# Kernel tuning notes

Measured on AMD Instinct MI355X. Metric: run time of the kernel, lower is better.

## Reference

```python
import jax, jax.numpy as jnp
import numpy as np

N = 100000      # nodes
E = 3200000     # edges
F_IN = 128      # num_features
H = 32          # hidden_dim (hard-coded in module)
C = 8           # num_classes
B = 128         # graphs in batch
BN_EPS = 1e-5


def setup_inputs() -> dict:
    key = jax.random.key(0)
    ks = jax.random.split(key, 24)
    s = 0.1
    inp = {
        "x": jax.random.normal(ks[0], (N, F_IN), jnp.float32),
        "edge_index": jax.random.randint(ks[1], (2, E), 0, N, dtype=jnp.int32),
        "batch": jnp.sort(jax.random.randint(ks[2], (N,), 0, B, dtype=jnp.int32)),
        # GINConv layer 0 (F_IN -> H -> H) MLP + BN params
        "w1_0": jax.random.normal(ks[3], (F_IN, H), jnp.float32) * s,
        "b1_0": jnp.zeros((H,), jnp.float32),
        "w2_0": jax.random.normal(ks[4], (H, H), jnp.float32) * s,
        "b2_0": jnp.zeros((H,), jnp.float32),
        "g_0": jnp.ones((H,), jnp.float32),
        "be_0": jnp.zeros((H,), jnp.float32),
        # GINConv layers 1..3 (H -> H -> H), stacked
        "w1s": jax.random.normal(ks[5], (3, H, H), jnp.float32) * s,
        "b1s": jnp.zeros((3, H), jnp.float32),
        "w2s": jax.random.normal(ks[6], (3, H, H), jnp.float32) * s,
        "b2s": jnp.zeros((3, H), jnp.float32),
        "gs": jnp.ones((3, H), jnp.float32),
        "bes": jnp.zeros((3, H), jnp.float32),
        # classifier head
        "fc1_w": jax.random.normal(ks[7], (H, H), jnp.float32) * s,
        "fc1_b": jnp.zeros((H,), jnp.float32),
        "fc2_w": jax.random.normal(ks[8], (H, C), jnp.float32) * s,
        "fc2_b": jnp.zeros((C,), jnp.float32),
    }
    return inp


def _gin_conv(h, src, dst, w1, b1, w2, b2):
    # GINConv with eps=0: MLP((1+eps)*x + sum_{j in N(i)} x_j)
    agg = jax.ops.segment_sum(h[src], dst, num_segments=N)  # scatter-add aggregation
    z = h + agg
    return jnp.maximum(z @ w1 + b1, 0.0) @ w2 + b2


def _batch_norm(h, gamma, beta):
    # BatchNorm1d in training mode: batch stats over node dim, biased variance
    mean = h.mean(axis=0)
    var = jnp.mean(jnp.square(h - mean), axis=0)
    return gamma * (h - mean) * jax.lax.rsqrt(var + BN_EPS) + beta


def reference(x, edge_index, batch, w1_0, b1_0, w2_0, b2_0, g_0, be_0,
              w1s, b1s, w2s, b2s, gs, bes, fc1_w, fc1_b, fc2_w, fc2_b):
    src, dst = edge_index[0], edge_index[1]
    h = _batch_norm(jnp.maximum(_gin_conv(x, src, dst, w1_0, b1_0, w2_0, b2_0), 0.0), g_0, be_0)
    for i in range(3):  # fixed small layer loop
        h = _batch_norm(jnp.maximum(_gin_conv(h, src, dst, w1s[i], b1s[i], w2s[i], b2s[i]), 0.0), gs[i], bes[i])
    # global_mean_pool over batch ids
    counts = jax.ops.segment_sum(jnp.ones((N,), h.dtype), batch, num_segments=B)
    pooled = jax.ops.segment_sum(h, batch, num_segments=B) / jnp.maximum(counts, 1.0)[:, None]
    h = jnp.maximum(pooled @ fc1_w + fc1_b, 0.0)
    # dropout p=0.5 treated as identity (eval-mode determinism)
    logits = h @ fc2_w + fc2_b
    return jax.nn.log_softmax(logits, axis=-1)
```

## Files before the change

### kernel.cpp

```cpp
#include <hip/hip_runtime.h>
#include <hip/hip_bf16.h>

#define NN   100000
#define EE   3200000
#define HH   32
#define BB   128
#define KMAX 96
#define LSTRIDE 97
#define NBKT 1024
#define BSPAN 98
#define EBLK 256
#define CHUNK 12500

typedef float f32x4 __attribute__((ext_vector_type(4)));

static constexpr size_t Q_OFF      = 0;
static constexpr size_t EPACK_OFF  = 6400000;
static constexpr size_t H_OFF      = 19200000;
static constexpr size_t SRC_OFF    = 32000000;
static constexpr size_t OFF_OFF    = 44800000;
static constexpr size_t HIST_OFF   = 45300000;
static constexpr size_t CUR_OFF    = 46400000;
static constexpr size_t BBASE_OFF  = 47500000;
static constexpr size_t STATS_OFF  = 47600000;
static constexpr size_t POOLED_OFF = 47601024;
static constexpr size_t PCNT_OFF   = 47617408;
static constexpr size_t TOTAL_OFF  = 47617920;
static constexpr size_t ZERO_OFF   = STATS_OFF;
static constexpr size_t ZERO_BYTES = 22016;

__global__ __launch_bounds__(256) void hist_kernel(const int* __restrict__ ei,
                                                   int* __restrict__ hist,
                                                   int* __restrict__ total) {
    __shared__ int lh[NBKT];
    int tid = threadIdx.x, blk = blockIdx.x;
    for (int i = tid; i < NBKT; i += 256) lh[i] = 0;
    __syncthreads();
    int e0 = blk * CHUNK;
    for (int e = e0 + tid; e < e0 + CHUNK; e += 256) {
        int d = ei[EE + e];
        atomicAdd(&lh[d / BSPAN], 1);
    }
    __syncthreads();
    for (int i = tid; i < NBKT; i += 256) {
        int c = lh[i];
        hist[blk * NBKT + i] = c;
        if (c > 0) atomicAdd(&total[i], c);
    }
}

__global__ __launch_bounds__(1024) void bucket_scan_kernel(const int* __restrict__ total,
                                                           int* __restrict__ bbase,
                                                           int* __restrict__ cursor) {
    __shared__ int sm[NBKT];
    int t = threadIdx.x;
    int mine = total[t];
    sm[t] = mine;
    __syncthreads();
    for (int off = 1; off < NBKT; off <<= 1) {
        int v = (t >= off) ? sm[t - off] : 0;
        __syncthreads();
        sm[t] += v;
        __syncthreads();
    }
    int base = sm[t] - mine;
    bbase[t] = base;
    cursor[t] = base;
    if (t == NBKT - 1) bbase[NBKT] = sm[t];
}

__global__ __launch_bounds__(256) void scatter_kernel(const int* __restrict__ ei,
                                                      const int* __restrict__ hist,
                                                      int* __restrict__ cursor,
                                                      int* __restrict__ epack) {
    __shared__ int lbs[NBKT];
    __shared__ int lh[NBKT];
    int tid = threadIdx.x, blk = blockIdx.x;
    for (int i = tid; i < NBKT; i += 256) {
        int c = hist[blk * NBKT + i];
        lbs[i] = (c > 0) ? atomicAdd(&cursor[i], c) : 0;
        lh[i] = 0;
    }
    __syncthreads();
    int e0 = blk * CHUNK;
    for (int e = e0 + tid; e < e0 + CHUNK; e += 256) {
        int s = ei[e];
        int d = ei[EE + e];
        int b = d / BSPAN;
        int slot = lbs[b] + atomicAdd(&lh[b], 1);
        epack[slot] = s | ((d - b * BSPAN) << 17);
    }
}

__global__ __launch_bounds__(256) void csr_compact_kernel(const int* __restrict__ epack,
                                                          const int* __restrict__ bbase,
                                                          int* __restrict__ off,
                                                          int* __restrict__ srcs) {
    __shared__ int lcnt[BSPAN];
    __shared__ int lbase[BSPAN + 1];
    __shared__ int lcsr[BSPAN * LSTRIDE];
    int b = blockIdx.x;
    int base = b * BSPAN;
    int span = NN - base;
    if (span <= 0) return;
    if (span > BSPAN) span = BSPAN;
    int tid = threadIdx.x;
    for (int i = tid; i < span; i += 256) lcnt[i] = 0;
    __syncthreads();
    int p0 = bbase[b], p1 = bbase[b + 1];
    for (int i = p0 + tid; i < p1; i += 256) {
        int wd = epack[i];
        int ld = wd >> 17;
        int slot = atomicAdd(&lcnt[ld], 1);
        if (slot < KMAX) lcsr[ld * LSTRIDE + slot] = wd & 0x1FFFF;
    }
    __syncthreads();
    if (tid == 0) {
        int run = 0;
        for (int i = 0; i < span; i++) { lbase[i] = run; run += min(lcnt[i], KMAX); }
        lbase[span] = run;
    }
    __syncthreads();
    for (int i = tid; i < span; i += 256) off[base + i] = p0 + lbase[i];
    if (base + span == NN && tid == 0) off[NN] = p0 + lbase[span];
    int m = lbase[span];
    for (int j = tid; j < m; j += 256) {
        int lo = 0, hi = span - 1;
        while (lo < hi) {
            int mid = (lo + hi + 1) >> 1;
            if (lbase[mid] <= j) lo = mid; else hi = mid - 1;
        }
        srcs[p0 + j] = lcsr[lo * LSTRIDE + (j - lbase[lo])];
    }
}

__device__ __forceinline__ unsigned bf16rn(float f) {
    unsigned b = __float_as_uint(f);
    return (b + 0x7fffu + ((b >> 16) & 1u)) >> 16;
}

__device__ __forceinline__ void acc_row(float* a, uint4 v) {
    a[0] += __uint_as_float(v.x << 16);
    a[1] += __uint_as_float(v.x & 0xffff0000u);
    a[2] += __uint_as_float(v.y << 16);
    a[3] += __uint_as_float(v.y & 0xffff0000u);
    a[4] += __uint_as_float(v.z << 16);
    a[5] += __uint_as_float(v.z & 0xffff0000u);
    a[6] += __uint_as_float(v.w << 16);
    a[7] += __uint_as_float(v.w & 0xffff0000u);
}

template <int FIN>
__global__ __launch_bounds__(256) void proj_kernel(const float* __restrict__ hin,
                                                   const float* __restrict__ w1,
                                                   const float* __restrict__ stats_prev,
                                                   const float* __restrict__ gamma,
                                                   const float* __restrict__ beta,
                                                   uint4* __restrict__ q4) {
    constexpr int JC = FIN / 4;
    __shared__ float sa[32], sc[32];
    __shared__ float part[4 * 64 * 33];
    int tid = threadIdx.x;
    if constexpr (FIN == 32) {
        if (tid < 32) {
            float mean = stats_prev[tid] * (1.0f / NN);
            float var  = fmaxf(stats_prev[32 + tid] * (1.0f / NN) - mean * mean, 0.f);
            float av = gamma[tid] * rsqrtf(var + 1e-5f);
            sa[tid] = av;
            sc[tid] = beta[tid] - mean * av;
        }
        __syncthreads();
    }
    int wv = __builtin_amdgcn_readfirstlane(tid >> 6);
    int ln = tid & 63;
    int n = blockIdx.x * 64 + ln;
    float acc[32];
#pragma unroll
    for (int c = 0; c < 32; c++) acc[c] = 0.f;
    if (n < NN) {
        const float4* h4 = (const float4*)(hin + (size_t)n * FIN + wv * JC);
        float hv[JC];
#pragma unroll
        for (int k = 0; k < JC / 4; k++) {
            float4 v = h4[k];
            hv[4*k] = v.x; hv[4*k+1] = v.y; hv[4*k+2] = v.z; hv[4*k+3] = v.w;
        }
        if constexpr (FIN == 32) {
#pragma unroll
            for (int j = 0; j < JC; j++) hv[j] = fmaf(hv[j], sa[wv * JC + j], sc[wv * JC + j]);
        }
#pragma unroll 4
        for (int j = 0; j < JC; j++) {
            float hvj = hv[j];
            const float* wrow = w1 + (size_t)(wv * JC + j) * 32;
#pragma unroll
            for (int c = 0; c < 32; c++) acc[c] = fmaf(hvj, wrow[c], acc[c]);
        }
    }
    float* my = part + (wv * 64 + ln) * 33;
#pragma unroll
    for (int c = 0; c < 32; c++) my[c] = acc[c];
    __syncthreads();
    int node = tid >> 2, p = tid & 3;
    int n2 = blockIdx.x * 64 + node;
    if (n2 >= NN) return;
    float r[8];
#pragma unroll
    for (int k = 0; k < 8; k++) {
        int c = p * 8 + k;
        r[k] = (part[(0 * 64 + node) * 33 + c] + part[(1 * 64 + node) * 33 + c])
             + (part[(2 * 64 + node) * 33 + c] + part[(3 * 64 + node) * 33 + c]);
    }
    uint4 u;
    u.x = bf16rn(r[0]) | (bf16rn(r[1]) << 16);
    u.y = bf16rn(r[2]) | (bf16rn(r[3]) << 16);
    u.z = bf16rn(r[4]) | (bf16rn(r[5]) << 16);
    u.w = bf16rn(r[6]) | (bf16rn(r[7]) << 16);
    q4[(size_t)n2 * 4 + p] = u;
}

__global__ __launch_bounds__(256) void gather_mlp_kernel(const uint4* __restrict__ q4,
                                                         const int* __restrict__ srcs,
                                                         const int* __restrict__ off,
                                                         const float* __restrict__ b1,
                                                         const float* __restrict__ w2,
                                                         const float* __restrict__ b2,
                                                         float* __restrict__ hout,
                                                         float* __restrict__ stats) {
    __shared__ float w2t[32 * 33];
    __shared__ float ut[64 * 33];
    __shared__ float pst[16 * 16];
    int tid = threadIdx.x;
    for (int i = tid; i < 1024; i += 256) w2t[(i >> 5) * 33 + (i & 31)] = w2[i];
    int t = blockIdx.x * 256 + tid;
    int n = t >> 2;
    int p = tid & 3;
    int node64 = tid >> 2;
    bool valid = (n < NN);
    float a[8];
#pragma unroll
    for (int k = 0; k < 8; k++) a[k] = valid ? b1[p * 8 + k] : 0.f;
    if (valid) {
        acc_row(a, q4[(size_t)n * 4 + p]);
        int o0 = off[n];
        int d = off[n + 1] - o0;
        const int* lst = srcs + o0;
        int i = 0;
        for (; i + 8 <= d; i += 8) {
            int s0 = __builtin_nontemporal_load(lst + i);
            int s1 = __builtin_nontemporal_load(lst + i + 1);
            int s2 = __builtin_nontemporal_load(lst + i + 2);
            int s3 = __builtin_nontemporal_load(lst + i + 3);
            int s4 = __builtin_nontemporal_load(lst + i + 4);
            int s5 = __builtin_nontemporal_load(lst + i + 5);
            int s6 = __builtin_nontemporal_load(lst + i + 6);
            int s7 = __builtin_nontemporal_load(lst + i + 7);
            uint4 v0 = q4[(size_t)s0 * 4 + p];
            uint4 v1 = q4[(size_t)s1 * 4 + p];
            uint4 v2 = q4[(size_t)s2 * 4 + p];
            uint4 v3 = q4[(size_t)s3 * 4 + p];
            uint4 v4 = q4[(size_t)s4 * 4 + p];
            uint4 v5 = q4[(size_t)s5 * 4 + p];
            uint4 v6 = q4[(size_t)s6 * 4 + p];
            uint4 v7 = q4[(size_t)s7 * 4 + p];
            acc_row(a, v0); acc_row(a, v1); acc_row(a, v2); acc_row(a, v3);
            acc_row(a, v4); acc_row(a, v5); acc_row(a, v6); acc_row(a, v7);
        }
        for (; i < d; i++) {
            int s = __builtin_nontemporal_load(lst + i);
            acc_row(a, q4[(size_t)s * 4 + p]);
        }
    }
    float* urow = ut + node64 * 33 + p * 8;
#pragma unroll
    for (int k = 0; k < 8; k++) urow[k] = fmaxf(a[k], 0.f);
    __syncthreads();
    int base = p * 8;
    float o[8];
#pragma unroll
    for (int k = 0; k < 8; k++) o[k] = valid ? b2[base + k] : 0.f;
    const float* un = ut + node64 * 33;
#pragma unroll 8
    for (int j = 0; j < 32; j++) {
        float uj = un[j];
        const float* wr = w2t + j * 33 + base;
#pragma unroll
        for (int k = 0; k < 8; k++) o[k] = fmaf(uj, wr[k], o[k]);
    }
#pragma unroll
    for (int k = 0; k < 8; k++) o[k] = fmaxf(o[k], 0.f);
    if (valid) {
        f32x4 h0, h1;
        h0.x = o[0]; h0.y = o[1]; h0.z = o[2]; h0.w = o[3];
        h1.x = o[4]; h1.y = o[5]; h1.z = o[6]; h1.w = o[7];
        f32x4* hr = (f32x4*)(hout + (size_t)n * 32 + base);
        __builtin_nontemporal_store(h0, hr);
        __builtin_nontemporal_store(h1, hr + 1);
    } else {
#pragma unroll
        for (int k = 0; k < 8; k++) o[k] = 0.f;
    }
    float s[8], q[8];
#pragma unroll
    for (int k = 0; k < 8; k++) { s[k] = o[k]; q[k] = o[k] * o[k]; }
#pragma unroll
    for (int m = 4; m < 64; m <<= 1) {
#pragma unroll
        for (int k = 0; k < 8; k++) {
            s[k] += __shfl_xor(s[k], m);
            q[k] += __shfl_xor(q[k], m);
        }
    }
    int wv = tid >> 6;
    if ((tid & 63) < 4) {
        float* ps = pst + (wv * 4 + p) * 16;
#pragma unroll
        for (int k = 0; k < 8; k++) { ps[k] = s[k]; ps[8 + k] = q[k]; }
    }
    __syncthreads();
    if (tid < 64) {
        int c = tid & 31;
        int issq = tid >> 5;
        int psel = c >> 3, k = c & 7;
        float acc = 0.f;
#pragma unroll
        for (int w = 0; w < 4; w++) acc += pst[(w * 4 + psel) * 16 + issq * 8 + k];
        atomicAdd(&stats[issq * 32 + c], acc);
    }
}

#define PR 16
__global__ __launch_bounds__(256) void pool_kernel(const float* __restrict__ h,
                                                   const int* __restrict__ batch,
                                                   float* __restrict__ pooled,
                                                   float* __restrict__ pcnt) {
    int t = blockIdx.x * 256 + threadIdx.x;
    int c = t & 31;
    int g = t >> 5;
    int r0 = g * PR;
    if (r0 >= NN) return;
    int r1 = min(r0 + PR, NN);
    int cur = batch[r0];
    float acc = 0.f, cn = 0.f;
    for (int rr = r0; rr < r1; rr++) {
        int b = batch[rr];
        if (b != cur) {
            atomicAdd(&pooled[cur * 32 + c], acc);
            if (c == 0) atomicAdd(&pcnt[cur], cn);
            acc = 0.f; cn = 0.f; cur = b;
        }
        acc += h[(size_t)rr * 32 + c];
        cn += 1.f;
    }
    atomicAdd(&pooled[cur * 32 + c], acc);
    if (c == 0) atomicAdd(&pcnt[cur], cn);
}

__global__ __launch_bounds__(128) void head_kernel(const float* __restrict__ pooled,
                                                   const float* __restrict__ pcnt,
                                                   const float* __restrict__ stats3,
                                                   const float* __restrict__ g3,
                                                   const float* __restrict__ be3,
                                                   const float* __restrict__ fc1w,
                                                   const float* __restrict__ fc1b,
                                                   const float* __restrict__ fc2w,
                                                   const float* __restrict__ fc2b,
                                                   float* __restrict__ out) {
    __shared__ float sa[32], sc[32];
    int g = threadIdx.x;
    if (g < 32) {
        float mean = stats3[g] * (1.0f / NN);
        float var  = fmaxf(stats3[32 + g] * (1.0f / NN) - mean * mean, 0.f);
        float av = g3[g] * rsqrtf(var + 1e-5f);
        sa[g] = av;
        sc[g] = be3[g] - mean * av;
    }
    __syncthreads();
    if (g >= BB) return;
    float inv = 1.f / fmaxf(pcnt[g], 1.f);
    float xv[32];
#pragma unroll
    for (int c = 0; c < 32; c++) xv[c] = fmaf(sa[c], pooled[g * 32 + c] * inv, sc[c]);
    float u[32];
#pragma unroll 4
    for (int k = 0; k < 32; k++) {
        float s = fc1b[k];
#pragma unroll
        for (int c = 0; c < 32; c++) s = fmaf(xv[c], fc1w[c * 32 + k], s);
        u[k] = fmaxf(s, 0.f);
    }
    float l[8];
#pragma unroll
    for (int o = 0; o < 8; o++) {
        float s = fc2b[o];
#pragma unroll
        for (int k = 0; k < 32; k++) s = fmaf(u[k], fc2w[k * 8 + o], s);
        l[o] = s;
    }
    float m = l[0];
#pragma unroll
    for (int o = 1; o < 8; o++) m = fmaxf(m, l[o]);
    float se = 0.f;
#pragma unroll
    for (int o = 0; o < 8; o++) se += expf(l[o] - m);
    float lse = logf(se) + m;
#pragma unroll
    for (int o = 0; o < 8; o++) out[g * 8 + o] = l[o] - lse;
}

extern "C" void kernel_launch(void* const* d_in, const int* in_sizes, int n_in,
                              void* d_out, int out_size, void* d_ws, size_t ws_size,
                              hipStream_t stream) {
    const float* x    = (const float*)d_in[0];
    const int*   ei   = (const int*)d_in[1];
    const int*   batch= (const int*)d_in[2];
    const float* w1_0 = (const float*)d_in[3];
    const float* b1_0 = (const float*)d_in[4];
    const float* w2_0 = (const float*)d_in[5];
    const float* b2_0 = (const float*)d_in[6];
    const float* g_0  = (const float*)d_in[7];
    const float* be_0 = (const float*)d_in[8];
    const float* w1s  = (const float*)d_in[9];
    const float* b1s  = (const float*)d_in[10];
    const float* w2s  = (const float*)d_in[11];
    const float* b2s  = (const float*)d_in[12];
    const float* gs   = (const float*)d_in[13];
    const float* bes  = (const float*)d_in[14];
    const float* fc1w = (const float*)d_in[15];
    const float* fc1b = (const float*)d_in[16];
    const float* fc2w = (const float*)d_in[17];
    const float* fc2b = (const float*)d_in[18];
    float* out = (float*)d_out;

    char* ws = (char*)d_ws;
    uint4*    q4     = (uint4*)(ws + Q_OFF);
    int*      epack  = (int*)(ws + EPACK_OFF);
    float*    h      = (float*)(ws + H_OFF);
    int*      srcs   = (int*)(ws + SRC_OFF);
    int*      off    = (int*)(ws + OFF_OFF);
    int*      hist   = (int*)(ws + HIST_OFF);
    int*      cursor = (int*)(ws + CUR_OFF);
    int*      bbase  = (int*)(ws + BBASE_OFF);
    float*    stats  = (float*)(ws + STATS_OFF);
    float*    pooled = (float*)(ws + POOLED_OFF);
    float*    pcnt   = (float*)(ws + PCNT_OFF);
    int*      total  = (int*)(ws + TOTAL_OFF);

    (void)hipMemsetAsync(ws + ZERO_OFF, 0, ZERO_BYTES, stream);

    hist_kernel<<<EBLK, 256, 0, stream>>>(ei, hist, total);
    bucket_scan_kernel<<<1, NBKT, 0, stream>>>(total, bbase, cursor);
    scatter_kernel<<<EBLK, 256, 0, stream>>>(ei, hist, cursor, epack);
    csr_compact_kernel<<<NBKT, 256, 0, stream>>>(epack, bbase, off, srcs);

    const int pblk = (NN + 63) / 64;
    const int gblk = (NN * 4 + 255) / 256;

    proj_kernel<128><<<pblk, 256, 0, stream>>>(x, w1_0, nullptr, nullptr, nullptr, q4);
    gather_mlp_kernel<<<gblk, 256, 0, stream>>>(q4, srcs, off, b1_0, w2_0, b2_0, h, stats);

    for (int i = 0; i < 3; i++) {
        const float* st_prev = stats + i * 64;
        proj_kernel<32><<<pblk, 256, 0, stream>>>(h, w1s + i * 1024, st_prev,
                                                  gs + i * 32, bes + i * 32, q4);
        gather_mlp_kernel<<<gblk, 256, 0, stream>>>(q4, srcs, off, b1s + i * 32,
                                                    w2s + i * 1024, b2s + i * 32, h,
                                                    stats + (i + 1) * 64);
    }

    int pthreads = ((NN + PR - 1) / PR) * 32;
    pool_kernel<<<(pthreads + 255) / 256, 256, 0, stream>>>(h, batch, pooled, pcnt);
    head_kernel<<<1, 128, 0, stream>>>(pooled, pcnt, stats + 3 * 64, gs + 2 * 32,
                                       bes + 2 * 32, fc1w, fc1b, fc2w, fc2b, out);
}
```

Before: 540.1 us.

## Stage bucket scatter in shared memory for coalesced epack writes

```diff
diff --git a/kernel.cpp b/kernel.cpp
--- a/kernel.cpp
+++ b/kernel.cpp
@@ -11,6 +11,7 @@
 #define BSPAN 98
 #define EBLK 256
 #define CHUNK 12500
+#define SBT  512
 
 typedef float f32x4 __attribute__((ext_vector_type(4)));
 
@@ -69,26 +70,51 @@
     if (t == NBKT - 1) bbase[NBKT] = sm[t];
 }
 
-__global__ __launch_bounds__(256) void scatter_kernel(const int* __restrict__ ei,
+__global__ __launch_bounds__(SBT) void scatter_kernel(const int* __restrict__ ei,
                                                       const int* __restrict__ hist,
                                                       int* __restrict__ cursor,
                                                       int* __restrict__ epack) {
+    __shared__ int st[CHUNK];
     __shared__ int lbs[NBKT];
-    __shared__ int lh[NBKT];
+    __shared__ int lbase[NBKT + 1];
+    __shared__ int lrun[NBKT];
+    __shared__ int psum[SBT];
     int tid = threadIdx.x, blk = blockIdx.x;
-    for (int i = tid; i < NBKT; i += 256) {
-        int c = hist[blk * NBKT + i];
-        lbs[i] = (c > 0) ? atomicAdd(&cursor[i], c) : 0;
-        lh[i] = 0;
-    }
+    int b0 = 2 * tid, b1 = 2 * tid + 1;
+    int c0 = hist[blk * NBKT + b0];
+    int c1 = hist[blk * NBKT + b1];
+    psum[tid] = c0 + c1;
+    __syncthreads();
+    for (int off = 1; off < SBT; off <<= 1) {
+        int v = (tid >= off) ? psum[tid - off] : 0;
+        __syncthreads();
+        psum[tid] += v;
+        __syncthreads();
+    }
+    int base = psum[tid] - (c0 + c1);
+    lbase[b0] = base;
+    lbase[b1] = base + c0;
+    if (tid == SBT - 1) lbase[NBKT] = psum[tid];
+    lrun[b0] = 0; lrun[b1] = 0;
+    lbs[b0] = c0 ? atomicAdd(&cursor[b0], c0) : 0;
+    lbs[b1] = c1 ? atomicAdd(&cursor[b1], c1) : 0;
     __syncthreads();
     int e0 = blk * CHUNK;
-    for (int e = e0 + tid; e < e0 + CHUNK; e += 256) {
+    for (int e = e0 + tid; e < e0 + CHUNK; e += SBT) {
         int s = ei[e];
         int d = ei[EE + e];
         int b = d / BSPAN;
-        int slot = lbs[b] + atomicAdd(&lh[b], 1);
-        epack[slot] = s | ((d - b * BSPAN) << 17);
+        int slot = lbase[b] + atomicAdd(&lrun[b], 1);
+        st[slot] = s | ((d - b * BSPAN) << 17);
+    }
+    __syncthreads();
+    for (int j = tid; j < CHUNK; j += SBT) {
+        int lo = 0, hi = NBKT - 1;
+        while (lo < hi) {
+            int mid = (lo + hi + 1) >> 1;
+            if (lbase[mid] <= j) lo = mid; else hi = mid - 1;
+        }
+        epack[lbs[lo] + (j - lbase[lo])] = st[j];
     }
 }
 
@@ -450,7 +476,7 @@
 
     hist_kernel<<<EBLK, 256, 0, stream>>>(ei, hist, total);
     bucket_scan_kernel<<<1, NBKT, 0, stream>>>(total, bbase, cursor);
-    scatter_kernel<<<EBLK, 256, 0, stream>>>(ei, hist, cursor, epack);
+    scatter_kernel<<<EBLK, SBT, 0, stream>>>(ei, hist, cursor, epack);
     csr_compact_kernel<<<NBKT, 256, 0, stream>>>(epack, bbase, off, srcs);
 
     const int pblk = (NN + 63) / 64;
```

Result: no change. 539.7 us (-0.1%).
